# Kernel optimization log

Measured on AMD Instinct MI355X. Metric: run time of the kernel, lower is better.

## Reference

```python
import jax, jax.numpy as jnp
import numpy as np

EMBED = 768
SPAT, TEMP, SYNC, GLOB, NEXP = 128, 64, 32, 64, 6


def _delta(x):
    # delta_i = x_i - x_{i-1}, with delta_0 = 0 (x_0 - x_0)
    x_shift = jnp.concatenate([x[:, :1, :], x[:, :-1, :]], axis=1)
    return x - x_shift


def setup_inputs() -> dict:
    key = jax.random.key(0)
    ks = jax.random.split(key, 13)
    B, S, D = 8, 4096, EMBED
    lim = lambda fan_in: 1.0 / np.sqrt(fan_in)
    u = lambda k, shp, fan_in: jax.random.uniform(k, shp, jnp.float32, -lim(fan_in), lim(fan_in))
    return {
        "x_text": jax.random.normal(ks[0], (B, S, D), jnp.float32),
        "x_au": jax.random.normal(ks[1], (B, S, D), jnp.float32),
        "x_vis": jax.random.normal(ks[2], (B, S, D), jnp.float32),
        "W_spat": u(ks[3], (3 * D, SPAT), 3 * D),
        "b_spat": u(ks[4], (SPAT,), 3 * D),
        "W_temp": u(ks[5], (3 * D, TEMP), 3 * D),
        "b_temp": u(ks[6], (TEMP,), 3 * D),
        "W_sync": u(ks[7], (D, SYNC), D),
        "b_sync": u(ks[8], (SYNC,), D),
        "W_glob": u(ks[9], (SPAT + TEMP + SYNC, GLOB), SPAT + TEMP + SYNC),
        "b_glob": u(ks[10], (GLOB,), SPAT + TEMP + SYNC),
        "W_route": u(ks[11], (SPAT + TEMP + SYNC + GLOB, NEXP), SPAT + TEMP + SYNC + GLOB),
        "b_route": u(ks[12], (NEXP,), SPAT + TEMP + SYNC + GLOB),
    }


def reference(x_text, x_au, x_vis, W_spat, b_spat, W_temp, b_temp,
              W_sync, b_sync, W_glob, b_glob, W_route, b_route):
    B, S, D = x_text.shape
    # local spatial: cat(text, au, vis) @ W_spat  -> (B,S,SPAT)
    spat_in = jnp.concatenate([x_text, x_au, x_vis], axis=-1)
    local_spat = jnp.einsum('bsf,fo->bso', spat_in, W_spat) + b_spat
    # local temporal: cat of first-order deltas -> (B,S,TEMP)
    temp_in = jnp.concatenate([_delta(x_text), _delta(x_au), _delta(x_vis)], axis=-1)
    local_temp = jnp.einsum('bsf,fo->bso', temp_in, W_temp) + b_temp
    # local sync: (au - vis) proj -> (B,S,SYNC)
    local_sync = jnp.einsum('bsf,fo->bso', x_au - x_vis, W_sync) + b_sync
    local_vec = jnp.concatenate([local_spat, local_temp, local_sync], axis=-1)
    # global context: mean over sequence of each local stream, then proj
    global_summary = jnp.mean(local_vec, axis=1)  # == cat of per-stream means
    global_vec = global_summary @ W_glob + b_glob  # (B,GLOB)
    # broadcast-concat + route projection
    glob_exp = jnp.broadcast_to(global_vec[:, None, :], (B, S, global_vec.shape[-1]))
    final_feat = jnp.concatenate([local_vec, glob_exp], axis=-1)
    gate_logits = jnp.einsum('bsf,fo->bso', final_feat, W_route) + b_route
    return gate_logits.reshape(-1, W_route.shape[-1])
```

## Files before the change

### kernel.cpp

```cpp
#include <hip/hip_runtime.h>

#define DIM 768
#define TD 2304
#define NB 8
#define NS 4096
#define NE 6

typedef __attribute__((ext_vector_type(8))) short bf16x8;
typedef __attribute__((ext_vector_type(4))) float f32x4;

#define OFF_BPK    0
#define OFF_A2F    36864
#define OFF_CB0    50688
#define OFF_ACCSUM 50704
#define OFF_CONSTB 50768
#define OFF_QP2    50832

__device__ __forceinline__ unsigned short f2bf(float f) {
    union { float f; unsigned u; } a; a.f = f;
    unsigned r = a.u + 0x7FFFu + ((a.u >> 16) & 1u);
    return (unsigned short)(r >> 16);
}

__global__ __launch_bounds__(256) void k_fold(
    const float* __restrict__ Wspat, const float* __restrict__ Wtemp,
    const float* __restrict__ Wsync, const float* __restrict__ Wroute,
    const float* __restrict__ Wglob, const float* __restrict__ bglob,
    const float* __restrict__ broute, const float* __restrict__ bspat,
    const float* __restrict__ btemp, const float* __restrict__ bsync,
    unsigned short* __restrict__ Bpk, float* __restrict__ A2F,
    float* __restrict__ cb0, float* __restrict__ accsum)
{
    __shared__ float lwr[288 * NE];
    __shared__ float lgf[224 * NE];
    const int t = threadIdx.x;
    for (int i = t; i < 288 * NE; i += 256) lwr[i] = Wroute[i];
    __syncthreads();
    if (t < 224) {
        float g[NE] = {0, 0, 0, 0, 0, 0};
        for (int o = 0; o < 64; ++o) {
            const float w = Wglob[t * 64 + o];
            #pragma unroll
            for (int e = 0; e < NE; ++e) g[e] += w * lwr[(224 + o) * NE + e];
        }
        #pragma unroll
        for (int e = 0; e < NE; ++e) lgf[t * NE + e] = g[e];
    }
    __syncthreads();
    if (blockIdx.x == 0) {
        if (t < NE) {
            float a = broute[t];
            for (int o = 0; o < 64; ++o)  a += bglob[o] * lwr[(224 + o) * NE + t];
            for (int o = 0; o < 128; ++o) a += bspat[o] * (lwr[o * NE + t] + lgf[o * NE + t]);
            for (int o = 0; o < 64; ++o)  a += btemp[o] * (lwr[(128 + o) * NE + t] + lgf[(128 + o) * NE + t]);
            for (int o = 0; o < 32; ++o)  a += bsync[o] * (lwr[(192 + o) * NE + t] + lgf[(192 + o) * NE + t]);
            cb0[t] = a;
        }
        if (t >= 128 && t < 192) accsum[t - 128] = 0.f;
    }

    const int d = blockIdx.x * 256 + t;
    const int st = d / DIM, dd = d - st * DIM;

    float p[NE] = {0, 0, 0, 0, 0, 0}, a2[NE] = {0, 0, 0, 0, 0, 0};
    for (int o = 0; o < 64; ++o) {
        const float w = Wtemp[d * 64 + o];
        #pragma unroll
        for (int e = 0; e < NE; ++e) {
            p[e]  += w * lwr[(128 + o) * NE + e];
            a2[e] += w * lgf[(128 + o) * NE + e];
        }
    }
    float qq[NE], a1[NE];
    #pragma unroll
    for (int e = 0; e < NE; ++e) { qq[e] = p[e]; a1[e] = 0.f; }
    for (int o = 0; o < 128; ++o) {
        const float w = Wspat[d * 128 + o];
        #pragma unroll
        for (int e = 0; e < NE; ++e) {
            qq[e] += w * lwr[o * NE + e];
            a1[e] += w * lgf[o * NE + e];
        }
    }
    if (st != 0) {
        const float sg = (st == 1) ? 1.f : -1.f;
        for (int o = 0; o < 32; ++o) {
            const float w = sg * Wsync[dd * 32 + o];
            #pragma unroll
            for (int e = 0; e < NE; ++e) {
                qq[e] += w * lwr[(192 + o) * NE + e];
                a1[e] += w * lgf[(192 + o) * NE + e];
            }
        }
    }
    const int ks = d >> 5, kk = d & 31;
    const int lh = (kk >> 3) * 16, j = kk & 7;
    unsigned short* b0 = Bpk + ks * 1024 + j;
    unsigned short* b1 = b0 + 512;
    #pragma unroll
    for (int e = 0; e < NE; ++e) {
        b0[(lh + e) * 8]     = f2bf(qq[e]);
        b0[(lh + 6 + e) * 8] = f2bf(p[e]);
        b1[(lh + e) * 8]     = f2bf(a1[e]);
        A2F[d * NE + e] = a2[e];
    }
}


#define GLOAD(C) { \
    const int gc0 = (khalf * 18 + (C)) * 64; \
    const int st_ = gc0 / DIM; \
    const float* Xp_ = (st_ == 0) ? xt : ((st_ == 1) ? xa : xv); \
    const float* Xr = Xp_ + (size_t)(rb0 + rloc) * DIM + (gc0 - st_ * DIM) + o * 8; \
    g0 = *(const float4*)(Xr);       g1 = *(const float4*)(Xr + 4); \
    g2 = *(const float4*)(Xr + DIM); g3 = *(const float4*)(Xr + DIM + 4); }

#define BLOAD(C, B00, B01, B10, B11) { \
    const unsigned short* bp = Bpk + ((khalf * 18 + (C)) << 11) + (l << 3); \
    B00 = *(const bf16x8*)(bp); \
    B01 = *(const bf16x8*)(bp + 512); \
    B10 = *(const bf16x8*)(bp + 1024); \
    B11 = *(const bf16x8*)(bp + 1536); }

#define STAGE(DB) { \
    bf16x8 v0, v1; \
    v0[0] = (short)f2bf(g0.x); v0[1] = (short)f2bf(g0.y); \
    v0[2] = (short)f2bf(g0.z); v0[3] = (short)f2bf(g0.w); \
    v0[4] = (short)f2bf(g1.x); v0[5] = (short)f2bf(g1.y); \
    v0[6] = (short)f2bf(g1.z); v0[7] = (short)f2bf(g1.w); \
    v1[0] = (short)f2bf(g2.x); v1[1] = (short)f2bf(g2.y); \
    v1[2] = (short)f2bf(g2.z); v1[3] = (short)f2bf(g2.w); \
    v1[4] = (short)f2bf(g3.x); v1[5] = (short)f2bf(g3.y); \
    v1[6] = (short)f2bf(g3.z); v1[7] = (short)f2bf(g3.w); \
    *(bf16x8*)&abuf[(DB) * 4096 + woff]     = v0; \
    *(bf16x8*)&abuf[(DB) * 4096 + woff + 8] = v1; }

#define COMPUTE(DB) { \
    const bf16x8 A0 = *(const bf16x8*)&abuf[(DB) * 4096 + (w * 512) + (l << 3)]; \
    const bf16x8 A1 = *(const bf16x8*)&abuf[(DB) * 4096 + 2048 + (w * 512) + (l << 3)]; \
    acc0 = __builtin_amdgcn_mfma_f32_16x16x32_bf16(A0, Bc00, acc0, 0, 0, 0); \
    acc1 = __builtin_amdgcn_mfma_f32_16x16x32_bf16(A0, Bc01, acc1, 0, 0, 0); \
    acc0 = __builtin_amdgcn_mfma_f32_16x16x32_bf16(A1, Bc10, acc0, 0, 0, 0); \
    acc1 = __builtin_amdgcn_mfma_f32_16x16x32_bf16(A1, Bc11, acc1, 0, 0, 0); }

__global__ __launch_bounds__(256, 4) void k_main(
    const float* __restrict__ xt, const float* __restrict__ xa, const float* __restrict__ xv,
    const unsigned short* __restrict__ Bpk, float* __restrict__ accsum,
    float* __restrict__ qp2)
{
    __shared__ unsigned short abuf[2 * 8 * 512];
    const int t = threadIdx.x;
    const int l = t & 63;
    const int w = t >> 6;
    const int bid = blockIdx.x;
    const int khalf = bid & 1;
    const int rblk = bid >> 1;
    const int rb0 = rblk << 6;
    const int bb = rblk >> 6;

    const int o = t & 7;
    const int rloc = (t >> 3) * 2;
    const int woff = (((o >> 2) * 4 + (rloc >> 4)) * 64 + (o & 3) * 16 + (rloc & 15)) * 8;

    f32x4 acc0 = {0.f, 0.f, 0.f, 0.f};
    f32x4 acc1 = {0.f, 0.f, 0.f, 0.f};
    float4 g0, g1, g2, g3;
    bf16x8 Bc00, Bc01, Bc10, Bc11, Bn00, Bn01, Bn10, Bn11;

    GLOAD(0)
    BLOAD(0, Bc00, Bc01, Bc10, Bc11)
    STAGE(0)
    __syncthreads();

    int db = 0;
    #pragma unroll 1
    for (int c = 0; c < 18; ++c) {
        if (c < 17) { GLOAD(c + 1) BLOAD(c + 1, Bn00, Bn01, Bn10, Bn11) }
        COMPUTE(db)
        __syncthreads();
        if (c < 17) {
            STAGE(db ^ 1)
            Bc00 = Bn00; Bc01 = Bn01; Bc10 = Bn10; Bc11 = Bn11;
            __syncthreads();
            db ^= 1;
        }
    }

    const int c_out = l & 15, rgrp = l >> 4;
    float* qph = qp2 + (size_t)khalf * ((size_t)NB * NS * 12);
    if (c_out < 12) {
        const size_t rbase = (size_t)(rb0 + w * 16 + rgrp * 4) * 12 + c_out;
        qph[rbase]      = acc0[0];
        qph[rbase + 12] = acc0[1];
        qph[rbase + 24] = acc0[2];
        qph[rbase + 36] = acc0[3];
    }
    float v = acc1[0] + acc1[1] + acc1[2] + acc1[3];
    v += __shfl_xor(v, 16, 64);
    v += __shfl_xor(v, 32, 64);
    if (rgrp == 0 && c_out < 6)
        atomicAdd(&accsum[bb * NE + c_out], v);
}

__global__ __launch_bounds__(256) void k_const(
    const float* __restrict__ xt, const float* __restrict__ xa, const float* __restrict__ xv,
    const float* __restrict__ accsum, const float* __restrict__ A2F,
    const float* __restrict__ cb0, float* __restrict__ constb)
{
    const int b = blockIdx.x, t = threadIdx.x;
    float acc[NE] = {0, 0, 0, 0, 0, 0};
    for (int f = t; f < TD; f += 256) {
        const int st = f / DIM, dd = f - st * DIM;
        const float* Xp = ((st == 0) ? xt : ((st == 1) ? xa : xv)) + (size_t)b * NS * DIM;
        const float dm = Xp[(size_t)(NS - 1) * DIM + dd] - Xp[dd];
        const float* Ap = A2F + f * NE;
        #pragma unroll
        for (int e = 0; e < NE; ++e) acc[e] += dm * Ap[e];
    }
    #pragma unroll
    for (int e = 0; e < NE; ++e)
        for (int m = 1; m < 64; m <<= 1) acc[e] += __shfl_xor(acc[e], m, 64);
    __shared__ float wred[4][NE];
    if ((t & 63) == 0) {
        #pragma unroll
        for (int e = 0; e < NE; ++e) wred[t >> 6][e] = acc[e];
    }
    __syncthreads();
    if (t < NE) {
        const float inv = 1.f / 4096.f;
        const float dsum = wred[0][t] + wred[1][t] + wred[2][t] + wred[3][t];
        constb[b * NE + t] = cb0[t] + accsum[b * NE + t] * inv + dsum * inv;
    }
}

__global__ __launch_bounds__(256) void k_add(
    const float* __restrict__ qp2, const float* __restrict__ constb, float* __restrict__ out)
{
    const int row = blockIdx.x * 256 + threadIdx.x;
    const int b = row >> 12, s = row & (NS - 1);
    const int rowp = (s == 0) ? row : row - 1;
    const size_t H = (size_t)NB * NS * 12;
    const float* q0 = qp2 + (size_t)row * 12;
    const float* q1 = qp2 + H + (size_t)row * 12;
    const float* p0 = qp2 + (size_t)rowp * 12 + 6;
    const float* p1 = qp2 + H + (size_t)rowp * 12 + 6;
    float* op = out + (size_t)row * NE;
    #pragma unroll
    for (int e = 0; e < NE; ++e)
        op[e] = constb[b * NE + e] + q0[e] + q1[e] - p0[e] - p1[e];
}

extern "C" void kernel_launch(void* const* d_in, const int* in_sizes, int n_in,
                              void* d_out, int out_size, void* d_ws, size_t ws_size,
                              hipStream_t stream)
{
    const float* xt     = (const float*)d_in[0];
    const float* xa     = (const float*)d_in[1];
    const float* xv     = (const float*)d_in[2];
    const float* Wspat  = (const float*)d_in[3];
    const float* bspat  = (const float*)d_in[4];
    const float* Wtemp  = (const float*)d_in[5];
    const float* btemp  = (const float*)d_in[6];
    const float* Wsync  = (const float*)d_in[7];
    const float* bsync  = (const float*)d_in[8];
    const float* Wglob  = (const float*)d_in[9];
    const float* bglob  = (const float*)d_in[10];
    const float* Wroute = (const float*)d_in[11];
    const float* broute = (const float*)d_in[12];
    float* out = (float*)d_out;

    float* ws = (float*)d_ws;
    unsigned short* Bpk = (unsigned short*)(ws + OFF_BPK);
    float* A2F    = ws + OFF_A2F;
    float* cb0    = ws + OFF_CB0;
    float* accsum = ws + OFF_ACCSUM;
    float* constb = ws + OFF_CONSTB;
    float* qp2    = ws + OFF_QP2;

    hipMemsetAsync(Bpk, 0, 73728 * sizeof(unsigned short), stream);
    k_fold<<<9, 256, 0, stream>>>(Wspat, Wtemp, Wsync, Wroute, Wglob, bglob,
                                  broute, bspat, btemp, bsync, Bpk, A2F, cb0, accsum);
    k_main<<<1024, 256, 0, stream>>>(xt, xa, xv, Bpk, accsum, qp2);
    k_const<<<8, 256, 0, stream>>>(xt, xa, xv, accsum, A2F, cb0, constb);
    k_add<<<128, 256, 0, stream>>>(qp2, constb, out);
}
```

Measured before the change: 119.9 us.

## Load A fragments directly from global into registers, drop LDS staging and barriers

The main GEMM kernel no longer stages the fp32 activations through shared memory. Each lane now loads its own MFMA A-fragment straight from global memory and converts it to bf16 in registers using the packed bf16 conversion intrinsic. A two-deep register prefetch replaces the LDS double buffer and removes both __syncthreads per chunk. The cost is more live registers, and each lane's global loads are less coalesced, now strided across rows instead of contiguous.

New measurement: 114.6 us. -4.4%, faster.

```diff
diff --git a/kernel.cpp b/kernel.cpp
--- a/kernel.cpp
+++ b/kernel.cpp
@@ -1,4 +1,5 @@
 #include <hip/hip_runtime.h>
+#include <hip/hip_bf16.h>
 
 #define DIM 768
 #define TD 2304
@@ -20,6 +21,15 @@
     union { float f; unsigned u; } a; a.f = f;
     unsigned r = a.u + 0x7FFFu + ((a.u >> 16) & 1u);
     return (unsigned short)(r >> 16);
+}
+
+__device__ __forceinline__ bf16x8 pack8(float4 a, float4 b) {
+    union { bf16x8 v; __hip_bfloat162 h[4]; } u;
+    u.h[0] = __float22bfloat162_rn(make_float2(a.x, a.y));
+    u.h[1] = __float22bfloat162_rn(make_float2(a.z, a.w));
+    u.h[2] = __float22bfloat162_rn(make_float2(b.x, b.y));
+    u.h[3] = __float22bfloat162_rn(make_float2(b.z, b.w));
+    return u.v;
 }
 
 __global__ __launch_bounds__(256) void k_fold(
@@ -107,13 +117,13 @@
 }
 
 
-#define GLOAD(C) { \
-    const int gc0 = (khalf * 18 + (C)) * 64; \
-    const int st_ = gc0 / DIM; \
+#define GLOADX(A0, A1, A2, A3, C) { \
+    const int gc_ = khalf * 1152 + (C) * 64; \
+    const int st_ = gc_ / DIM; \
     const float* Xp_ = (st_ == 0) ? xt : ((st_ == 1) ? xa : xv); \
-    const float* Xr = Xp_ + (size_t)(rb0 + rloc) * DIM + (gc0 - st_ * DIM) + o * 8; \
-    g0 = *(const float4*)(Xr);       g1 = *(const float4*)(Xr + 4); \
-    g2 = *(const float4*)(Xr + DIM); g3 = *(const float4*)(Xr + DIM + 4); }
+    const float* Xr_ = Xp_ + rowoff + (gc_ - st_ * DIM); \
+    A0 = *(const float4*)(Xr_);      A1 = *(const float4*)(Xr_ + 4); \
+    A2 = *(const float4*)(Xr_ + 32); A3 = *(const float4*)(Xr_ + 36); }
 
 #define BLOAD(C, B00, B01, B10, B11) { \
     const unsigned short* bp = Bpk + ((khalf * 18 + (C)) << 11) + (l << 3); \
@@ -122,33 +132,19 @@
     B10 = *(const bf16x8*)(bp + 1024); \
     B11 = *(const bf16x8*)(bp + 1536); }
 
-#define STAGE(DB) { \
-    bf16x8 v0, v1; \
-    v0[0] = (short)f2bf(g0.x); v0[1] = (short)f2bf(g0.y); \
-    v0[2] = (short)f2bf(g0.z); v0[3] = (short)f2bf(g0.w); \
-    v0[4] = (short)f2bf(g1.x); v0[5] = (short)f2bf(g1.y); \
-    v0[6] = (short)f2bf(g1.z); v0[7] = (short)f2bf(g1.w); \
-    v1[0] = (short)f2bf(g2.x); v1[1] = (short)f2bf(g2.y); \
-    v1[2] = (short)f2bf(g2.z); v1[3] = (short)f2bf(g2.w); \
-    v1[4] = (short)f2bf(g3.x); v1[5] = (short)f2bf(g3.y); \
-    v1[6] = (short)f2bf(g3.z); v1[7] = (short)f2bf(g3.w); \
-    *(bf16x8*)&abuf[(DB) * 4096 + woff]     = v0; \
-    *(bf16x8*)&abuf[(DB) * 4096 + woff + 8] = v1; }
-
-#define COMPUTE(DB) { \
-    const bf16x8 A0 = *(const bf16x8*)&abuf[(DB) * 4096 + (w * 512) + (l << 3)]; \
-    const bf16x8 A1 = *(const bf16x8*)&abuf[(DB) * 4096 + 2048 + (w * 512) + (l << 3)]; \
-    acc0 = __builtin_amdgcn_mfma_f32_16x16x32_bf16(A0, Bc00, acc0, 0, 0, 0); \
-    acc1 = __builtin_amdgcn_mfma_f32_16x16x32_bf16(A0, Bc01, acc1, 0, 0, 0); \
-    acc0 = __builtin_amdgcn_mfma_f32_16x16x32_bf16(A1, Bc10, acc0, 0, 0, 0); \
-    acc1 = __builtin_amdgcn_mfma_f32_16x16x32_bf16(A1, Bc11, acc1, 0, 0, 0); }
+#define CMPT(A0, A1, A2, A3, B00, B01, B10, B11) { \
+    const bf16x8 fA0 = pack8(A0, A1); \
+    const bf16x8 fA1 = pack8(A2, A3); \
+    acc0 = __builtin_amdgcn_mfma_f32_16x16x32_bf16(fA0, B00, acc0, 0, 0, 0); \
+    acc1 = __builtin_amdgcn_mfma_f32_16x16x32_bf16(fA0, B01, acc1, 0, 0, 0); \
+    acc0 = __builtin_amdgcn_mfma_f32_16x16x32_bf16(fA1, B10, acc0, 0, 0, 0); \
+    acc1 = __builtin_amdgcn_mfma_f32_16x16x32_bf16(fA1, B11, acc1, 0, 0, 0); }
 
 __global__ __launch_bounds__(256, 4) void k_main(
     const float* __restrict__ xt, const float* __restrict__ xa, const float* __restrict__ xv,
     const unsigned short* __restrict__ Bpk, float* __restrict__ accsum,
     float* __restrict__ qp2)
 {
-    __shared__ unsigned short abuf[2 * 8 * 512];
     const int t = threadIdx.x;
     const int l = t & 63;
     const int w = t >> 6;
@@ -158,33 +154,31 @@
     const int rb0 = rblk << 6;
     const int bb = rblk >> 6;
 
-    const int o = t & 7;
-    const int rloc = (t >> 3) * 2;
-    const int woff = (((o >> 2) * 4 + (rloc >> 4)) * 64 + (o & 3) * 16 + (rloc & 15)) * 8;
+    const int arow = rb0 + w * 16 + (l & 15);
+    const size_t rowoff = (size_t)arow * DIM + (l >> 4) * 8;
 
     f32x4 acc0 = {0.f, 0.f, 0.f, 0.f};
     f32x4 acc1 = {0.f, 0.f, 0.f, 0.f};
-    float4 g0, g1, g2, g3;
-    bf16x8 Bc00, Bc01, Bc10, Bc11, Bn00, Bn01, Bn10, Bn11;
-
-    GLOAD(0)
-    BLOAD(0, Bc00, Bc01, Bc10, Bc11)
-    STAGE(0)
-    __syncthreads();
-
-    int db = 0;
+
+    float4 pa0, pa1, pa2, pa3, pb0, pb1, pb2, pb3;
+    bf16x8 Ba00, Ba01, Ba10, Ba11, Bb00, Bb01, Bb10, Bb11;
+
+    GLOADX(pa0, pa1, pa2, pa3, 0)
+    BLOAD(0, Ba00, Ba01, Ba10, Ba11)
+    GLOADX(pb0, pb1, pb2, pb3, 1)
+    BLOAD(1, Bb00, Bb01, Bb10, Bb11)
+
     #pragma unroll 1
-    for (int c = 0; c < 18; ++c) {
-        if (c < 17) { GLOAD(c + 1) BLOAD(c + 1, Bn00, Bn01, Bn10, Bn11) }
-        COMPUTE(db)
-        __syncthreads();
-        if (c < 17) {
-            STAGE(db ^ 1)
-            Bc00 = Bn00; Bc01 = Bn01; Bc10 = Bn10; Bc11 = Bn11;
-            __syncthreads();
-            db ^= 1;
-        }
-    }
+    for (int c = 0; c < 16; c += 2) {
+        CMPT(pa0, pa1, pa2, pa3, Ba00, Ba01, Ba10, Ba11)
+        GLOADX(pa0, pa1, pa2, pa3, c + 2)
+        BLOAD(c + 2, Ba00, Ba01, Ba10, Ba11)
+        CMPT(pb0, pb1, pb2, pb3, Bb00, Bb01, Bb10, Bb11)
+        GLOADX(pb0, pb1, pb2, pb3, c + 3)
+        BLOAD(c + 3, Bb00, Bb01, Bb10, Bb11)
+    }
+    CMPT(pa0, pa1, pa2, pa3, Ba00, Ba01, Ba10, Ba11)
+    CMPT(pb0, pb1, pb2, pb3, Bb00, Bb01, Bb10, Bb11)
 
     const int c_out = l & 15, rgrp = l >> 4;
     float* qph = qp2 + (size_t)khalf * ((size_t)NB * NS * 12);
```
